# Kernel tuning notes

Hardware: AMD Instinct MI355X
Metric: run time of the kernel (lower is better)

The kernel has to match this reference:

```python
import jax, jax.numpy as jnp
import numpy as np

EPS = 1e-05

def setup_inputs() -> dict:
    key = jax.random.key(0)
    inputs = jax.random.normal(key, (32, 512, 768), dtype=jnp.float32)
    return {"inputs": inputs}

def reference(inputs) -> jnp.ndarray:
    # position weight: L2 norm per token, w[b,l] = sqrt(1e-5 + sum_d x^2)
    w = jnp.sqrt(EPS + jnp.sum(inputs * inputs, axis=-1))  # [B, L]
    # output[b,d,e] = sum_l w[b,l] * x[b,l,d] * x[b,l,e]
    # fused weighted Gram matrix; never materializes [B,L,D,D]
    return jnp.einsum('bld,ble->bde', inputs * w[..., None], inputs)
```

## Files before the change

kernel.cpp:

```cpp
#include <hip/hip_runtime.h>
#include <hip/hip_bf16.h>

#define BATCH 32
#define LL 512
#define DD 768
#define EPSC 1e-5f

typedef __attribute__((ext_vector_type(8))) short bf16x8;
typedef __attribute__((ext_vector_type(4))) float f32x4;

__global__ __launch_bounds__(256) void k_prep(const float* __restrict__ x,
                                              ushort* __restrict__ yt) {
    __shared__ float tile[64][65];
    __shared__ float svec[64];
    int lb = blockIdx.x;
    int b = blockIdx.y;
    int l0 = lb * 64;
    int t = threadIdx.x;

    {
        int r = t >> 2, q = t & 3;
        const float4* xr = (const float4*)(x + ((size_t)b * LL + l0 + r) * DD) + q * 48;
        float sum = 0.f;
#pragma unroll 8
        for (int i = 0; i < 48; i++) {
            float4 v = xr[i];
            sum += v.x * v.x + v.y * v.y + v.z * v.z + v.w * v.w;
        }
        sum += __shfl_xor(sum, 1, 64);
        sum += __shfl_xor(sum, 2, 64);
        if (q == 0) svec[r] = sqrtf(sqrtf(EPSC + sum));
    }
    __syncthreads();

    const float* xb = x + ((size_t)b * LL + l0) * DD;
    int f = t & 15, lr0 = t >> 4;
    int lc = t & 7, dl0 = t >> 3;
    for (int dt = 0; dt < 12; dt++) {
        int d0 = dt * 64;
#pragma unroll
        for (int r = 0; r < 4; r++) {
            int l = lr0 + r * 16;
            float4 v = *(const float4*)(xb + (size_t)l * DD + d0 + f * 4);
#pragma unroll
            for (int j = 0; j < 4; j++)
                tile[l][f * 4 + j] = ((const float*)&v)[j];
        }
        __syncthreads();
        ushort* yp = yt + ((size_t)b * DD + d0) * LL + l0;
#pragma unroll
        for (int it = 0; it < 2; it++) {
            int d = dl0 + it * 32;
            bf16x8 w;
#pragma unroll
            for (int j = 0; j < 8; j++) {
                int l = lc * 8 + j;
                float v = tile[l][d] * svec[l];
                __hip_bfloat16 h = __float2bfloat16(v);
                w[j] = *(short*)&h;
            }
            *(bf16x8*)(yp + (size_t)d * LL + lc * 8) = w;
        }
        __syncthreads();
    }
}

__global__ __launch_bounds__(256) void k_gemm(const ushort* __restrict__ yt,
                                              float* __restrict__ out) {
    __shared__ ushort At[2][64 * 64];
    __shared__ ushort Bt[2][64 * 64];
    int i = blockIdx.x;
    int xcd = i & 7, slot = i >> 3;
    int b = xcd + 8 * (slot / 78);
    int p = slot % 78;
    int t = p, tm = 0, rem = 12;
    while (t >= rem) { t -= rem; rem--; tm++; }
    int tn = tm + t;
    bool diag = (tm == tn);
    int m0 = tm * 64, n0 = tn * 64;
    int tid = threadIdx.x;
    int wave = tid >> 6, lane = tid & 63;
    int wr = wave >> 1, wc = wave & 1;
    const ushort* yb = yt + (size_t)b * DD * LL;

    f32x4 acc[2][2];
#pragma unroll
    for (int ii = 0; ii < 2; ii++)
#pragma unroll
        for (int j = 0; j < 2; j++) acc[ii][j] = (f32x4){0.f, 0.f, 0.f, 0.f};

    int s0 = tid, s1 = 256 + tid;
    int sr0 = s0 >> 3, sc0 = (s0 & 7) ^ (sr0 & 7);
    int sr1 = s1 >> 3, sc1 = (s1 & 7) ^ (sr1 & 7);
    const ushort* gA0 = yb + (size_t)(m0 + sr0) * LL + sc0 * 8;
    const ushort* gA1 = yb + (size_t)(m0 + sr1) * LL + sc1 * 8;
    const ushort* gB0 = yb + (size_t)(n0 + sr0) * LL + sc0 * 8;
    const ushort* gB1 = yb + (size_t)(n0 + sr1) * LL + sc1 * 8;
    int ldsOff0 = (0 * 256 + wave * 64) * 8;
    int ldsOff1 = (1 * 256 + wave * 64) * 8;

    int fr = lane & 15, ks4 = lane >> 4;

#define STAGE(buf, ks) do {                                                   \
        int k0_ = (ks) * 64;                                                  \
        __builtin_amdgcn_global_load_lds(                                     \
            (const __attribute__((address_space(1))) void*)(gA0 + k0_),       \
            (__attribute__((address_space(3))) void*)(At[buf] + ldsOff0),     \
            16, 0, 0);                                                        \
        __builtin_amdgcn_global_load_lds(                                     \
            (const __attribute__((address_space(1))) void*)(gA1 + k0_),       \
            (__attribute__((address_space(3))) void*)(At[buf] + ldsOff1),     \
            16, 0, 0);                                                        \
        if (!diag) {                                                          \
            __builtin_amdgcn_global_load_lds(                                 \
                (const __attribute__((address_space(1))) void*)(gB0 + k0_),   \
                (__attribute__((address_space(3))) void*)(Bt[buf] + ldsOff0), \
                16, 0, 0);                                                    \
            __builtin_amdgcn_global_load_lds(                                 \
                (const __attribute__((address_space(1))) void*)(gB1 + k0_),   \
                (__attribute__((address_space(3))) void*)(Bt[buf] + ldsOff1), \
                16, 0, 0);                                                    \
        }                                                                     \
    } while (0)

    STAGE(0, 0);
    __syncthreads();
    for (int ks = 0; ks < 8; ks++) {
        int cur = ks & 1;
        if (ks < 7) STAGE(cur ^ 1, ks + 1);
        const ushort* Ab = At[cur];
        const ushort* Bb = diag ? At[cur] : Bt[cur];
        bf16x8 af[2][2], bf[2][2];
#pragma unroll
        for (int ii = 0; ii < 2; ii++) {
            int mr = wr * 32 + ii * 16 + fr;
            int nr = wc * 32 + ii * 16 + fr;
#pragma unroll
            for (int h = 0; h < 2; h++) {
                int slm = ((h * 4 + ks4) ^ (mr & 7)) * 8;
                int sln = ((h * 4 + ks4) ^ (nr & 7)) * 8;
                af[ii][h] = *(const bf16x8*)(Ab + mr * 64 + slm);
                bf[ii][h] = *(const bf16x8*)(Bb + nr * 64 + sln);
            }
        }
#pragma unroll
        for (int ii = 0; ii < 2; ii++)
#pragma unroll
            for (int j = 0; j < 2; j++)
#pragma unroll
                for (int h = 0; h < 2; h++)
                    acc[ii][j] = __builtin_amdgcn_mfma_f32_16x16x32_bf16(
                        af[ii][h], bf[j][h], acc[ii][j], 0, 0, 0);
        if (ks < 7) __syncthreads();
    }
#undef STAGE

    float* op = out + (size_t)b * DD * DD;
#pragma unroll
    for (int ii = 0; ii < 2; ii++) {
        int colb = m0 + wr * 32 + ii * 16 + (lane >> 4) * 4;
#pragma unroll
        for (int j = 0; j < 2; j++) {
            int row = n0 + wc * 32 + j * 16 + fr;
            float4 v = {acc[ii][j][0], acc[ii][j][1], acc[ii][j][2], acc[ii][j][3]};
            *(float4*)(op + (size_t)row * DD + colb) = v;
        }
    }
    if (!diag) {
#pragma unroll
        for (int ii = 0; ii < 2; ii++) {
            int mbase = m0 + wr * 32 + ii * 16 + (lane >> 4) * 4;
#pragma unroll
            for (int j = 0; j < 2; j++) {
                int n = n0 + wc * 32 + j * 16 + fr;
#pragma unroll
                for (int r = 0; r < 4; r++)
                    op[(size_t)(mbase + r) * DD + n] = acc[ii][j][r];
            }
        }
    }
}

extern "C" void kernel_launch(void* const* d_in, const int* in_sizes, int n_in,
                              void* d_out, int out_size, void* d_ws, size_t ws_size,
                              hipStream_t stream) {
    const float* x = (const float*)d_in[0];
    ushort* yt = (ushort*)d_ws;

    k_prep<<<dim3(LL / 64, BATCH), 256, 0, stream>>>(x, yt);
    k_gemm<<<dim3(78 * BATCH), 256, 0, stream>>>(yt, (float*)d_out);
}
```

Baseline: 130.8 us.

## Enlarge symmetric Gram GEMM tiles from 64x64 to 128x128

Each GEMM block now computes a 128x128 output tile, with every wave holding a 4x4 grid of MFMA accumulators instead of 2x2. The triangular tile count per batch drops from 78 to 21, and the staging loads are widened to fill the larger LDS tiles. This raises arithmetic intensity and cuts redundant global and LDS traffic. The cost is more registers and LDS per block and only 672 blocks, which may leave some CUs idle or unevenly loaded.

```diff
diff --git a/kernel.cpp b/kernel.cpp
--- a/kernel.cpp
+++ b/kernel.cpp
@@ -67,59 +67,63 @@
 
 __global__ __launch_bounds__(256) void k_gemm(const ushort* __restrict__ yt,
                                               float* __restrict__ out) {
-    __shared__ ushort At[2][64 * 64];
-    __shared__ ushort Bt[2][64 * 64];
+    __shared__ ushort At[2][128 * 64];
+    __shared__ ushort Bt[2][128 * 64];
     int i = blockIdx.x;
     int xcd = i & 7, slot = i >> 3;
-    int b = xcd + 8 * (slot / 78);
-    int p = slot % 78;
-    int t = p, tm = 0, rem = 12;
+    int b = xcd + 8 * (slot / 21);
+    int p = slot % 21;
+    int t = p, tm = 0, rem = 6;
     while (t >= rem) { t -= rem; rem--; tm++; }
     int tn = tm + t;
     bool diag = (tm == tn);
-    int m0 = tm * 64, n0 = tn * 64;
+    int m0 = tm * 128, n0 = tn * 128;
     int tid = threadIdx.x;
     int wave = tid >> 6, lane = tid & 63;
     int wr = wave >> 1, wc = wave & 1;
     const ushort* yb = yt + (size_t)b * DD * LL;
 
-    f32x4 acc[2][2];
+    f32x4 acc[4][4];
 #pragma unroll
-    for (int ii = 0; ii < 2; ii++)
+    for (int ii = 0; ii < 4; ii++)
 #pragma unroll
-        for (int j = 0; j < 2; j++) acc[ii][j] = (f32x4){0.f, 0.f, 0.f, 0.f};
+        for (int j = 0; j < 4; j++) acc[ii][j] = (f32x4){0.f, 0.f, 0.f, 0.f};
 
-    int s0 = tid, s1 = 256 + tid;
-    int sr0 = s0 >> 3, sc0 = (s0 & 7) ^ (sr0 & 7);
-    int sr1 = s1 >> 3, sc1 = (s1 & 7) ^ (sr1 & 7);
-    const ushort* gA0 = yb + (size_t)(m0 + sr0) * LL + sc0 * 8;
-    const ushort* gA1 = yb + (size_t)(m0 + sr1) * LL + sc1 * 8;
-    const ushort* gB0 = yb + (size_t)(n0 + sr0) * LL + sc0 * 8;
-    const ushort* gB1 = yb + (size_t)(n0 + sr1) * LL + sc1 * 8;
-    int ldsOff0 = (0 * 256 + wave * 64) * 8;
-    int ldsOff1 = (1 * 256 + wave * 64) * 8;
+    int sr[4], sc[4];
+#pragma unroll
+    for (int is = 0; is < 4; is++) {
+        int s = is * 256 + tid;
+        sr[is] = s >> 3;
+        sc[is] = (s & 7) ^ (sr[is] & 7);
+    }
+    const ushort* gA[4];
+    const ushort* gB[4];
+#pragma unroll
+    for (int is = 0; is < 4; is++) {
+        gA[is] = yb + (size_t)(m0 + sr[is]) * LL + sc[is] * 8;
+        gB[is] = yb + (size_t)(n0 + sr[is]) * LL + sc[is] * 8;
+    }
+    int ldsOff[4];
+#pragma unroll
+    for (int is = 0; is < 4; is++) ldsOff[is] = (is * 256 + wave * 64) * 8;
 
     int fr = lane & 15, ks4 = lane >> 4;
 
 #define STAGE(buf, ks) do {                                                   \
         int k0_ = (ks) * 64;                                                  \
-        __builtin_amdgcn_global_load_lds(                                     \
-            (const __attribute__((address_space(1))) void*)(gA0 + k0_),       \
-            (__attribute__((address_space(3))) void*)(At[buf] + ldsOff0),     \
-            16, 0, 0);                                                        \
-        __builtin_amdgcn_global_load_lds(                                     \
-            (const __attribute__((address_space(1))) void*)(gA1 + k0_),       \
-            (__attribute__((address_space(3))) void*)(At[buf] + ldsOff1),     \
-            16, 0, 0);                                                        \
+        _Pragma("unroll")                                                     \
+        for (int is = 0; is < 4; is++)                                        \
+            __builtin_amdgcn_global_load_lds(                                 \
+                (const __attribute__((address_space(1))) void*)(gA[is] + k0_),\
+                (__attribute__((address_space(3))) void*)(At[buf] + ldsOff[is]),\
+                16, 0, 0);                                                    \
         if (!diag) {                                                          \
-            __builtin_amdgcn_global_load_lds(                                 \
-                (const __attribute__((address_space(1))) void*)(gB0 + k0_),   \
-                (__attribute__((address_space(3))) void*)(Bt[buf] + ldsOff0), \
-                16, 0, 0);                                                    \
-            __builtin_amdgcn_global_load_lds(                                 \
-                (const __attribute__((address_space(1))) void*)(gB1 + k0_),   \
-                (__attribute__((address_space(3))) void*)(Bt[buf] + ldsOff1), \
-                16, 0, 0);                                                    \
+            _Pragma("unroll")                                                 \
+            for (int is = 0; is < 4; is++)                                    \
+                __builtin_amdgcn_global_load_lds(                             \
+                    (const __attribute__((address_space(1))) void*)(gB[is] + k0_),\
+                    (__attribute__((address_space(3))) void*)(Bt[buf] + ldsOff[is]),\
+                    16, 0, 0);                                                \
         }                                                                     \
     } while (0)
 
@@ -130,11 +134,11 @@
         if (ks < 7) STAGE(cur ^ 1, ks + 1);
         const ushort* Ab = At[cur];
         const ushort* Bb = diag ? At[cur] : Bt[cur];
-        bf16x8 af[2][2], bf[2][2];
+        bf16x8 af[4][2], bf[4][2];
 #pragma unroll
-        for (int ii = 0; ii < 2; ii++) {
-            int mr = wr * 32 + ii * 16 + fr;
-            int nr = wc * 32 + ii * 16 + fr;
+        for (int ii = 0; ii < 4; ii++) {
+            int mr = wr * 64 + ii * 16 + fr;
+            int nr = wc * 64 + ii * 16 + fr;
 #pragma unroll
             for (int h = 0; h < 2; h++) {
                 int slm = ((h * 4 + ks4) ^ (mr & 7)) * 8;
@@ -144,9 +148,9 @@
             }
         }
 #pragma unroll
-        for (int ii = 0; ii < 2; ii++)
+        for (int ii = 0; ii < 4; ii++)
 #pragma unroll
-            for (int j = 0; j < 2; j++)
+            for (int j = 0; j < 4; j++)
 #pragma unroll
                 for (int h = 0; h < 2; h++)
                     acc[ii][j] = __builtin_amdgcn_mfma_f32_16x16x32_bf16(
@@ -157,22 +161,22 @@
 
     float* op = out + (size_t)b * DD * DD;
 #pragma unroll
-    for (int ii = 0; ii < 2; ii++) {
-        int colb = m0 + wr * 32 + ii * 16 + (lane >> 4) * 4;
+    for (int ii = 0; ii < 4; ii++) {
+        int colb = m0 + wr * 64 + ii * 16 + ks4 * 4;
 #pragma unroll
-        for (int j = 0; j < 2; j++) {
-            int row = n0 + wc * 32 + j * 16 + fr;
+        for (int j = 0; j < 4; j++) {
+            int row = n0 + wc * 64 + j * 16 + fr;
             float4 v = {acc[ii][j][0], acc[ii][j][1], acc[ii][j][2], acc[ii][j][3]};
             *(float4*)(op + (size_t)row * DD + colb) = v;
         }
     }
     if (!diag) {
 #pragma unroll
-        for (int ii = 0; ii < 2; ii++) {
-            int mbase = m0 + wr * 32 + ii * 16 + (lane >> 4) * 4;
+        for (int ii = 0; ii < 4; ii++) {
+            int mbase = m0 + wr * 64 + ii * 16 + ks4 * 4;
 #pragma unroll
-            for (int j = 0; j < 2; j++) {
-                int n = n0 + wc * 32 + j * 16 + fr;
+            for (int j = 0; j < 4; j++) {
+                int n = n0 + wc * 64 + j * 16 + fr;
 #pragma unroll
                 for (int r = 0; r < 4; r++)
                     op[(size_t)(mbase + r) * DD + n] = acc[ii][j][r];
@@ -188,5 +192,5 @@
     ushort* yt = (ushort*)d_ws;
 
     k_prep<<<dim3(LL / 64, BATCH), 256, 0, stream>>>(x, yt);
-    k_gemm<<<dim3(78 * BATCH), 256, 0, stream>>>(yt, (float*)d_out);
+    k_gemm<<<dim3(21 * BATCH), 256, 0, stream>>>(yt, (float*)d_out);
 }
```

New measurement: 133.0 us. No clear change (+1.6%).
